# Kernel tuning notes

Hardware: AMD Instinct MI355X
Metric: run time of the kernel (lower is better)

## Reference

```python
import jax, jax.numpy as jnp
import numpy as np

V, E, G = 25000, 50000, 1024
D_IN, E_IN, D, EH = 74, 12, 64, 128
STEPS, S2S, L, NT = 6, 6, 3, 1


def setup_inputs() -> dict:
    key = jax.random.key(0)
    ks = jax.random.split(key, 20)
    p = lambda k, shp: (jax.random.normal(k, shp, jnp.float32) * 0.05)
    return {
        "node_feats": jax.random.normal(ks[0], (V, D_IN), jnp.float32),
        "edge_feats": jax.random.normal(ks[1], (E, E_IN), jnp.float32),
        "src": jax.random.randint(ks[2], (E,), 0, V),
        "dst": jax.random.randint(ks[3], (E,), 0, V),
        "node2graph": jnp.sort(jax.random.randint(ks[4], (V,), 0, G)),
        "W_proj": p(ks[5], (D_IN, D)), "b_proj": jnp.zeros((D,), jnp.float32),
        "W_e1": p(ks[6], (E_IN, EH)), "b_e1": jnp.zeros((EH,), jnp.float32),
        "W_e2": p(ks[7], (EH, D * D)), "b_e2": jnp.zeros((D * D,), jnp.float32),
        "b_conv": jnp.zeros((D,), jnp.float32),
        "gru_W_ih": p(ks[8], (3 * D, D)), "gru_W_hh": p(ks[9], (3 * D, D)),
        "gru_b_ih": jnp.zeros((3 * D,), jnp.float32), "gru_b_hh": jnp.zeros((3 * D,), jnp.float32),
        "lstm_W_ih0": p(ks[10], (4 * D, 2 * D)), "lstm_W_hh0": p(ks[11], (4 * D, D)),
        "lstm_b_ih0": jnp.zeros((4 * D,), jnp.float32), "lstm_b_hh0": jnp.zeros((4 * D,), jnp.float32),
        "lstm_W_ih_r": p(ks[12], (L - 1, 4 * D, D)), "lstm_W_hh_r": p(ks[13], (L - 1, 4 * D, D)),
        "lstm_b_ih_r": jnp.zeros((L - 1, 4 * D), jnp.float32), "lstm_b_hh_r": jnp.zeros((L - 1, 4 * D), jnp.float32),
        "W1": p(ks[14], (2 * D, D)), "b1": jnp.zeros((D,), jnp.float32),
        "bn_gamma": jnp.ones((D,), jnp.float32), "bn_beta": jnp.zeros((D,), jnp.float32),
        "bn_mean": jnp.zeros((D,), jnp.float32), "bn_var": jnp.ones((D,), jnp.float32),
        "W2": p(ks[15], (D, 4 * NT)), "b2": jnp.zeros((4 * NT,), jnp.float32),
    }


def reference(node_feats, edge_feats, src, dst, node2graph,
              W_proj, b_proj, W_e1, b_e1, W_e2, b_e2, b_conv,
              gru_W_ih, gru_W_hh, gru_b_ih, gru_b_hh,
              lstm_W_ih0, lstm_W_hh0, lstm_b_ih0, lstm_b_hh0,
              lstm_W_ih_r, lstm_W_hh_r, lstm_b_ih_r, lstm_b_hh_r,
              W1, b1, bn_gamma, bn_beta, bn_mean, bn_var, W2, b2):
    # --- MPNNGNN: project + ReLU, then NNConv(sum) + ReLU + GRU, x STEPS ---
    h = jax.nn.relu(node_feats @ W_proj + b_proj)                       # (V, D)
    # edge network: per-edge (D,D) mixing matrix (edge_feats constant across steps)
    We = (jax.nn.relu(edge_feats @ W_e1 + b_e1) @ W_e2 + b_e2).reshape(E, D, D)

    def mp_step(hh, _):
        m = jnp.einsum('ed,edo->eo', hh[src], We)                       # per-edge message
        agg = jax.ops.segment_sum(m, dst, num_segments=V) + b_conv      # NNConv sum + bias
        x = jax.nn.relu(agg)
        gi = x @ gru_W_ih.T + gru_b_ih                                  # GRU (torch gate order r,z,n)
        gh = hh @ gru_W_hh.T + gru_b_hh
        ir, iz, inn = jnp.split(gi, 3, axis=-1)
        hr, hz, hn = jnp.split(gh, 3, axis=-1)
        r = jax.nn.sigmoid(ir + hr)
        z = jax.nn.sigmoid(iz + hz)
        n = jnp.tanh(inn + r * hn)
        return (1.0 - z) * n + z * hh, None

    h, _ = jax.lax.scan(mp_step, h, None, length=STEPS)

    # --- Set2Set readout ---
    q_star = jnp.zeros((G, 2 * D), h.dtype)
    hs = jnp.zeros((L, G, D), h.dtype)
    cs = jnp.zeros((L, G, D), h.dtype)
    for _ in range(S2S):
        x = q_star
        nh, nc = [], []
        for l in range(L):                                              # stacked LSTM, seq len 1
            Wih = lstm_W_ih0 if l == 0 else lstm_W_ih_r[l - 1]
            Whh = lstm_W_hh0 if l == 0 else lstm_W_hh_r[l - 1]
            bih = lstm_b_ih0 if l == 0 else lstm_b_ih_r[l - 1]
            bhh = lstm_b_hh0 if l == 0 else lstm_b_hh_r[l - 1]
            gates = x @ Wih.T + bih + hs[l] @ Whh.T + bhh               # torch order i,f,g,o
            i, f, g, o = jnp.split(gates, 4, axis=-1)
            c = jax.nn.sigmoid(f) * cs[l] + jax.nn.sigmoid(i) * jnp.tanh(g)
            hc = jax.nn.sigmoid(o) * jnp.tanh(c)
            nh.append(hc); nc.append(c)
            x = hc
        hs, cs = jnp.stack(nh), jnp.stack(nc)
        q = x                                                           # (G, D)
        e = jnp.sum(h * q[node2graph], axis=-1)                         # (V,) attention logits
        emax = jax.lax.stop_gradient(jax.ops.segment_max(e, node2graph, num_segments=G))
        emax = jnp.where(jnp.isfinite(emax), emax, 0.0)
        ez = jnp.exp(e - emax[node2graph])                              # per-graph softmax
        denom = jax.ops.segment_sum(ez, node2graph, num_segments=G)
        alpha = ez / jnp.maximum(denom[node2graph], 1e-12)
        readout = jax.ops.segment_sum(h * alpha[:, None], node2graph, num_segments=G)
        q_star = jnp.concatenate([q, readout], axis=-1)                 # (G, 2D)

    # --- evidential head: Linear + ReLU + BatchNorm(eval) + Linear ---
    h1 = jax.nn.relu(q_star @ W1 + b1)
    hbn = bn_gamma * (h1 - bn_mean) * jax.lax.rsqrt(bn_var + 1e-5) + bn_beta
    out = hbn @ W2 + b2                                                 # (G, 4*NT)
    means, logl, loga, logb = jnp.split(out, 4, axis=1)
    MINV = 1e-6
    lam = jax.nn.softplus(logl) + MINV
    alp = jax.nn.softplus(loga) + MINV + 1.0
    bet = jax.nn.softplus(logb) + MINV
    return jnp.stack([means, lam, alp, bet], axis=2).reshape(out.shape)
```

## Files before the change

### kernel.cpp

```cpp
#include <hip/hip_runtime.h>
#include <stdint.h>

#define V_N 25000
#define E_N 50000
#define G_N 1024
#define DIN 74
#define EIN 12
#define NSTEPS 6
#define NS2S 6
#define MPAD 50048

typedef unsigned int u32;
typedef unsigned short u16;
typedef __attribute__((ext_vector_type(8))) short bf16x8v;
typedef __attribute__((ext_vector_type(4))) float f32x4v;

typedef __attribute__((address_space(3))) void lds_void;
typedef __attribute__((address_space(1))) void gbl_void;

__device__ __forceinline__ void gload_lds16(const void* g, void* l) {
  __builtin_amdgcn_global_load_lds((gbl_void*)g, (lds_void*)l, 16, 0, 0);
}

__device__ __forceinline__ u16 f2bf(float f) {
  u32 u = __float_as_uint(f);
  u = (u + 0x7fffu + ((u >> 16) & 1u)) >> 16;
  return (u16)u;
}
__device__ __forceinline__ u32 pack2bf(float lo, float hi) {
  return (u32)f2bf(lo) | ((u32)f2bf(hi) << 16);
}
__device__ __forceinline__ float bflo(u32 w){ return __uint_as_float(w << 16); }
__device__ __forceinline__ float bfhi(u32 w){ return __uint_as_float(w & 0xffff0000u); }
__device__ __forceinline__ float sigf(float x){ return 1.f/(1.f + expf(-x)); }
__device__ __forceinline__ float splusf(float x){ return fmaxf(x, 0.f) + log1pf(expf(-fabsf(x))); }

__global__ void prep_kernel(const float* gWih, const float* gWhh,
                            const float* lWih0, const float* lWhh0,
                            const float* lWihr, const float* lWhhr,
                            const float* We2,
                            float* gWihT, float* gWhhT,
                            u32* TW40, u32* TU40, u32* TW4r, u32* TU4r,
                            u16* WbT) {
  int idx = blockIdx.x * 256 + threadIdx.x;
  if (idx < 12288) { int d = idx / 192, r = idx % 192; gWihT[idx] = gWih[r*64 + d]; return; }
  idx -= 12288;
  if (idx < 12288) { int d = idx / 192, r = idx % 192; gWhhT[idx] = gWhh[r*64 + d]; return; }
  idx -= 12288;
  if (idx < 16384) { int q = idx >> 2, j = idx & 3; int k8 = q >> 8, r = q & 255;
                     TW40[idx] = pack2bf(lWih0[r*128 + k8*8 + 2*j], lWih0[r*128 + k8*8 + 2*j + 1]); return; }
  idx -= 16384;
  if (idx < 8192)  { int q = idx >> 2, j = idx & 3; int k8 = q >> 8, r = q & 255;
                     TU40[idx] = pack2bf(lWhh0[r*64 + k8*8 + 2*j], lWhh0[r*64 + k8*8 + 2*j + 1]); return; }
  idx -= 8192;
  if (idx < 16384) { int l = idx >> 13, rem = idx & 8191; int q = rem >> 2, j = rem & 3;
                     int k8 = q >> 8, r = q & 255;
                     TW4r[idx] = pack2bf(lWihr[l*16384 + r*64 + k8*8 + 2*j],
                                         lWihr[l*16384 + r*64 + k8*8 + 2*j + 1]); return; }
  idx -= 16384;
  if (idx < 16384) { int l = idx >> 13, rem = idx & 8191; int q = rem >> 2, j = rem & 3;
                     int k8 = q >> 8, r = q & 255;
                     TU4r[idx] = pack2bf(lWhhr[l*16384 + r*64 + k8*8 + 2*j],
                                         lWhhr[l*16384 + r*64 + k8*8 + 2*j + 1]); return; }
  idx -= 16384;
  { int n = idx / 128, k = idx % 128; WbT[idx] = f2bf(We2[k*4096 + n]); }
}

__global__ void proj_kernel(const float* nf, const float* Wp, const float* bp, float* h) {
  int v = blockIdx.x * 4 + (threadIdx.x >> 6);
  int o = threadIdx.x & 63;
  if (v >= V_N) return;
  float acc = bp[o];
  const float* row = nf + (size_t)v * DIN;
  #pragma unroll 2
  for (int d = 0; d < DIN; ++d) acc += row[d] * Wp[d*64 + o];
  h[(size_t)v*64 + o] = fmaxf(acc, 0.f);
}

__global__ void edgenet_kernel(const float* ef, const float* W1, const float* b1, u16* zb) {
  int e = blockIdx.x * 2 + (threadIdx.x >> 7);
  int k = threadIdx.x & 127;
  float acc = 0.f;
  if (e < E_N) {
    acc = b1[k];
    const float* row = ef + (size_t)e * EIN;
    #pragma unroll
    for (int i = 0; i < EIN; ++i) acc += row[i] * W1[i*128 + k];
    acc = fmaxf(acc, 0.f);
  }
  zb[(size_t)e*128 + k] = f2bf(acc);
}

__global__ __launch_bounds__(512) void fusedmsg_kernel(const u16* zb, const u16* WbT, const float* be2,
                                                       const float* h, const int* src, const int* dst,
                                                       float* agg) {
  __shared__ __align__(16) u16 Bs[2][8192];
  __shared__ float hS[128][66];
  int t = threadIdx.x;
  int e0 = blockIdx.x * 128;
  int w = t >> 6, lane = t & 63;
  int l16 = lane & 15, lh = lane >> 4;

  for (int it = 0; it < 16; ++it) {
    int idx = it * 512 + t;
    int el = idx >> 6, d = idx & 63;
    int e = e0 + el;
    int sv = (e < E_N) ? src[e] : 0;
    hS[el][d] = h[(size_t)sv * 64 + d];
  }

  bf16x8v af[4];
  #pragma unroll
  for (int ks = 0; ks < 4; ++ks)
    af[ks] = *(const bf16x8v*)(zb + (size_t)(e0 + w*16 + l16)*128 + ks*32 + lh*8);

  {
    const char* Bg = (const char*)WbT;
    char* Bl = (char*)Bs[0];
    #pragma unroll
    for (int it = 0; it < 2; ++it) {
      int f = it * 512 + t;
      int r = f >> 4, s = f & 15;
      int gc = s ^ (r & 7);
      gload_lds16(Bg + r*256 + gc*16, Bl + (size_t)(f & ~63) * 16);
    }
  }
  __syncthreads();

  float macc[4][4];
  #pragma unroll
  for (int of = 0; of < 4; ++of)
    #pragma unroll
    for (int r = 0; r < 4; ++r) macc[of][r] = 0.f;

  for (int d = 0; d < 64; ++d) {
    int buf = d & 1;
    if (d < 63) {
      const char* Bg = (const char*)WbT + (size_t)(d + 1) * 16384;
      char* Bl = (char*)Bs[buf ^ 1];
      #pragma unroll
      for (int it = 0; it < 2; ++it) {
        int f = it * 512 + t;
        int r = f >> 4, s = f & 15;
        int gc = s ^ (r & 7);
        gload_lds16(Bg + r*256 + gc*16, Bl + (size_t)(f & ~63) * 16);
      }
    }
    float hv[4];
    #pragma unroll
    for (int r = 0; r < 4; ++r) hv[r] = hS[w*16 + lh*4 + r][d];

    const char* Bb = (const char*)Bs[buf];
    #pragma unroll
    for (int of = 0; of < 4; ++of) {
      float bias = be2[d*64 + of*16 + l16];
      f32x4v c = (f32x4v){bias, bias, bias, bias};
      #pragma unroll
      for (int ks = 0; ks < 4; ++ks) {
        int brow = of*16 + l16;
        int cb = ks*4 + lh;
        bf16x8v bf = *(const bf16x8v*)(Bb + brow*256 + ((cb ^ (brow & 7)) << 4));
        c = __builtin_amdgcn_mfma_f32_16x16x32_bf16(af[ks], bf, c, 0, 0, 0);
      }
      #pragma unroll
      for (int r = 0; r < 4; ++r) macc[of][r] += hv[r] * c[r];
    }
    __syncthreads();
  }

  #pragma unroll
  for (int r = 0; r < 4; ++r) {
    int row = w*16 + lh*4 + r;
    int e = e0 + row;
    if (e < E_N) {
      int dv = dst[e];
      #pragma unroll
      for (int of = 0; of < 4; ++of)
        atomicAdd(&agg[(size_t)dv*64 + of*16 + l16], macc[of][r]);
    }
  }
}

__global__ void gru_kernel(const float* aggc, const float* bconv, const float* WihT, const float* WhhT,
                           const float* bih, const float* bhh, float* h, float* aggz) {
  int wbase = (blockIdx.x * 4 + (threadIdx.x >> 6)) * 4;
  int o = threadIdx.x & 63;
  float xv[4], hv[4];
  #pragma unroll
  for (int n = 0; n < 4; ++n) {
    int v = wbase + n;
    if (v < V_N) { xv[n] = fmaxf(aggc[(size_t)v*64 + o] + bconv[o], 0.f); hv[n] = h[(size_t)v*64 + o]; }
    else { xv[n] = 0.f; hv[n] = 0.f; }
  }
  float ar[4] = {0,0,0,0}, az[4] = {0,0,0,0}, an[4] = {0,0,0,0};
  float br[4] = {0,0,0,0}, bz[4] = {0,0,0,0}, bn2[4] = {0,0,0,0};
  #pragma unroll 4
  for (int d = 0; d < 64; ++d) {
    float wr = WihT[d*192 + o], wz = WihT[d*192 + 64 + o], wn = WihT[d*192 + 128 + o];
    float ur = WhhT[d*192 + o], uz = WhhT[d*192 + 64 + o], un = WhhT[d*192 + 128 + o];
    #pragma unroll
    for (int n = 0; n < 4; ++n) {
      float xd = __shfl(xv[n], d);
      float hd = __shfl(hv[n], d);
      ar[n] += xd*wr; az[n] += xd*wz; an[n] += xd*wn;
      br[n] += hd*ur; bz[n] += hd*uz; bn2[n] += hd*un;
    }
  }
  float b_r = bih[o] + bhh[o], b_z = bih[64+o] + bhh[64+o];
  float bin = bih[128+o], bhn = bhh[128+o];
  #pragma unroll
  for (int n = 0; n < 4; ++n) {
    int v = wbase + n;
    if (v >= V_N) continue;
    float r  = sigf(ar[n] + br[n] + b_r);
    float z  = sigf(az[n] + bz[n] + b_z);
    float nn = tanhf(an[n] + bin + r*(bn2[n] + bhn));
    h[(size_t)v*64 + o] = (1.f - z)*nn + z*hv[n];
    aggz[(size_t)v*64 + o] = 0.f;
  }
}

__global__ void gstart_kernel(const int* n2g, int* gstart) {
  int g = blockIdx.x * 256 + threadIdx.x;
  if (g > G_N) return;
  int lo = 0, hi = V_N;
  while (lo < hi) { int mid = (lo + hi) >> 1; if (n2g[mid] < g) lo = mid + 1; else hi = mid; }
  gstart[g] = lo;
}

__global__ __launch_bounds__(256) void s2s_kernel(const float* h, const int* gstart,
    const uint4* TW40, const uint4* TU40, const uint4* TW4r, const uint4* TU4r,
    const float* bih0, const float* bhh0, const float* bihr, const float* bhhr,
    float* qstar) {
  __shared__ float sq[4][128];
  __shared__ float sx[4][128];
  __shared__ float shs[4][3][64], scs[4][3][64];
  __shared__ float sg[4][256];
  int tt = threadIdx.x;
  int g0blk = blockIdx.x * 4;
  int w = tt >> 6, lane = tt & 63;
  int nstart = gstart[g0blk + w], nend = gstart[g0blk + w + 1];

  for (int i = tt; i < 512; i += 256) ((float*)sq)[i] = 0.f;
  for (int i = tt; i < 768; i += 256) { ((float*)shs)[i] = 0.f; ((float*)scs)[i] = 0.f; }
  __syncthreads();

  for (int iter = 0; iter < NS2S; ++iter) {
    for (int i = tt; i < 512; i += 256) ((float*)sx)[i] = ((float*)sq)[i];
    __syncthreads();

    for (int l = 0; l < 3; ++l) {
      const uint4* TW = (l == 0) ? TW40 : TW4r + (size_t)(l-1) * 2048;
      const uint4* TU = (l == 0) ? TU40 : TU4r + (size_t)(l-1) * 2048;
      const float* bi = (l == 0) ? bih0 : bihr + (l-1)*256;
      const float* bh = (l == 0) ? bhh0 : bhhr + (l-1)*256;
      float bsum = bi[tt] + bh[tt];
      float acc[4] = {bsum, bsum, bsum, bsum};
      if (l == 0) {
        #pragma unroll
        for (int k8 = 0; k8 < 16; ++k8) {
          uint4 u = TW[k8*256 + tt];
          #pragma unroll
          for (int gi = 0; gi < 4; ++gi) {
            const float4 xa = *(const float4*)&sx[gi][k8*8];
            const float4 xb = *(const float4*)&sx[gi][k8*8 + 4];
            acc[gi] += xa.x*bflo(u.x) + xa.y*bfhi(u.x) + xa.z*bflo(u.y) + xa.w*bfhi(u.y)
                     + xb.x*bflo(u.z) + xb.y*bfhi(u.z) + xb.z*bflo(u.w) + xb.w*bfhi(u.w);
          }
        }
      } else {
        #pragma unroll
        for (int k8 = 0; k8 < 8; ++k8) {
          uint4 u = TW[k8*256 + tt];
          #pragma unroll
          for (int gi = 0; gi < 4; ++gi) {
            const float4 xa = *(const float4*)&sx[gi][k8*8];
            const float4 xb = *(const float4*)&sx[gi][k8*8 + 4];
            acc[gi] += xa.x*bflo(u.x) + xa.y*bfhi(u.x) + xa.z*bflo(u.y) + xa.w*bfhi(u.y)
                     + xb.x*bflo(u.z) + xb.y*bfhi(u.z) + xb.z*bflo(u.w) + xb.w*bfhi(u.w);
          }
        }
      }
      #pragma unroll
      for (int k8 = 0; k8 < 8; ++k8) {
        uint4 u = TU[k8*256 + tt];
        #pragma unroll
        for (int gi = 0; gi < 4; ++gi) {
          const float4 ha = *(const float4*)&shs[gi][l][k8*8];
          const float4 hb = *(const float4*)&shs[gi][l][k8*8 + 4];
          acc[gi] += ha.x*bflo(u.x) + ha.y*bfhi(u.x) + ha.z*bflo(u.y) + ha.w*bfhi(u.y)
                   + hb.x*bflo(u.z) + hb.y*bfhi(u.z) + hb.z*bflo(u.w) + hb.w*bfhi(u.w);
        }
      }
      #pragma unroll
      for (int gi = 0; gi < 4; ++gi) sg[gi][tt] = acc[gi];
      __syncthreads();
      {
        int gq = tt >> 6, r = tt & 63;
        float gv_i = sg[gq][r], gv_f = sg[gq][64+r], gv_g = sg[gq][128+r], gv_o = sg[gq][192+r];
        float c = sigf(gv_f)*scs[gq][l][r] + sigf(gv_i)*tanhf(gv_g);
        float hc = sigf(gv_o)*tanhf(c);
        scs[gq][l][r] = c; shs[gq][l][r] = hc; sx[gq][r] = hc;
      }
      __syncthreads();
    }

    {
      float q_l = sx[w][lane];
      float lmax = -3.4e38f;
      int i = nstart;
      for (; i + 1 < nend; i += 2) {
        float h0 = h[(size_t)i*64 + lane];
        float h1 = h[(size_t)(i+1)*64 + lane];
        float v0 = h0 * q_l, v1 = h1 * q_l;
        #pragma unroll
        for (int off = 32; off; off >>= 1) { v0 += __shfl_xor(v0, off); v1 += __shfl_xor(v1, off); }
        lmax = fmaxf(lmax, fmaxf(v0, v1));
      }
      if (i < nend) {
        float h0 = h[(size_t)i*64 + lane];
        float v0 = h0 * q_l;
        #pragma unroll
        for (int off = 32; off; off >>= 1) v0 += __shfl_xor(v0, off);
        lmax = fmaxf(lmax, v0);
      }
      float lsum = 0.f, accv = 0.f;
      i = nstart;
      for (; i + 1 < nend; i += 2) {
        float h0 = h[(size_t)i*64 + lane];
        float h1 = h[(size_t)(i+1)*64 + lane];
        float v0 = h0 * q_l, v1 = h1 * q_l;
        #pragma unroll
        for (int off = 32; off; off >>= 1) { v0 += __shfl_xor(v0, off); v1 += __shfl_xor(v1, off); }
        float e0 = expf(v0 - lmax), e1 = expf(v1 - lmax);
        lsum += e0 + e1; accv += e0*h0 + e1*h1;
      }
      if (i < nend) {
        float h0 = h[(size_t)i*64 + lane];
        float v0 = h0 * q_l;
        #pragma unroll
        for (int off = 32; off; off >>= 1) v0 += __shfl_xor(v0, off);
        float e0 = expf(v0 - lmax);
        lsum += e0; accv += e0*h0;
      }
      sq[w][lane] = sx[w][lane];
      sq[w][64 + lane] = accv / fmaxf(lsum, 1e-12f);
    }
    __syncthreads();
  }

  for (int i = tt; i < 512; i += 256) qstar[(size_t)g0blk * 128 + i] = ((float*)sq)[i];
}

__global__ void head_kernel(const float* qstar, const float* W1, const float* b1,
                            const float* gma, const float* gbe, const float* gme, const float* gva,
                            const float* W2, const float* b2, float* out) {
  __shared__ float hb[4][64];
  int wslot = threadIdx.x >> 6;
  int g = blockIdx.x * 4 + wslot;
  int o = threadIdx.x & 63;
  float acc = b1[o];
  const float* q = qstar + (size_t)g * 128;
  #pragma unroll 4
  for (int k = 0; k < 128; ++k) acc += q[k] * W1[k*64 + o];
  acc = fmaxf(acc, 0.f);
  float hbn = gma[o] * (acc - gme[o]) * rsqrtf(gva[o] + 1e-5f) + gbe[o];
  hb[wslot][o] = hbn;
  __syncthreads();
  if (o < 4) {
    float v = b2[o];
    #pragma unroll 8
    for (int k = 0; k < 64; ++k) v += hb[wslot][k] * W2[k*4 + o];
    float res;
    if (o == 0) res = v;
    else { res = splusf(v) + 1e-6f; if (o == 2) res += 1.f; }
    out[(size_t)g*4 + o] = res;
  }
}

extern "C" void kernel_launch(void* const* d_in, const int* in_sizes, int n_in,
                              void* d_out, int out_size, void* d_ws, size_t ws_size,
                              hipStream_t stream) {
  const float* node_feats = (const float*)d_in[0];
  const float* edge_feats = (const float*)d_in[1];
  const int*   src        = (const int*)d_in[2];
  const int*   dst        = (const int*)d_in[3];
  const int*   n2g        = (const int*)d_in[4];
  const float* W_proj = (const float*)d_in[5];
  const float* b_proj = (const float*)d_in[6];
  const float* W_e1   = (const float*)d_in[7];
  const float* b_e1   = (const float*)d_in[8];
  const float* W_e2   = (const float*)d_in[9];
  const float* b_e2   = (const float*)d_in[10];
  const float* b_conv = (const float*)d_in[11];
  const float* gru_W_ih = (const float*)d_in[12];
  const float* gru_W_hh = (const float*)d_in[13];
  const float* gru_b_ih = (const float*)d_in[14];
  const float* gru_b_hh = (const float*)d_in[15];
  const float* lstm_W_ih0 = (const float*)d_in[16];
  const float* lstm_W_hh0 = (const float*)d_in[17];
  const float* lstm_b_ih0 = (const float*)d_in[18];
  const float* lstm_b_hh0 = (const float*)d_in[19];
  const float* lstm_W_ih_r = (const float*)d_in[20];
  const float* lstm_W_hh_r = (const float*)d_in[21];
  const float* lstm_b_ih_r = (const float*)d_in[22];
  const float* lstm_b_hh_r = (const float*)d_in[23];
  const float* W1 = (const float*)d_in[24];
  const float* b1 = (const float*)d_in[25];
  const float* bn_gamma = (const float*)d_in[26];
  const float* bn_beta  = (const float*)d_in[27];
  const float* bn_mean  = (const float*)d_in[28];
  const float* bn_var   = (const float*)d_in[29];
  const float* W2 = (const float*)d_in[30];
  const float* b2 = (const float*)d_in[31];

  char* ws = (char*)d_ws;
  size_t off = 0;
  auto alloc = [&](size_t n) { size_t c = off; off += (n + 255) & ~(size_t)255; return c; };
  u16*   zb     = (u16*)  (ws + alloc((size_t)MPAD * 128 * 2));
  float* h      = (float*)(ws + alloc((size_t)V_N * 64 * 4));
  float* agg    = (float*)(ws + alloc((size_t)V_N * 64 * 4));
  u16*   WbT    = (u16*)  (ws + alloc((size_t)4096 * 128 * 2));
  float* gWihT  = (float*)(ws + alloc(12288 * 4));
  float* gWhhT  = (float*)(ws + alloc(12288 * 4));
  u32*   TW40   = (u32*)  (ws + alloc(16384 * 4));
  u32*   TU40   = (u32*)  (ws + alloc(8192 * 4));
  u32*   TW4r   = (u32*)  (ws + alloc(16384 * 4));
  u32*   TU4r   = (u32*)  (ws + alloc(16384 * 4));
  int*   gstart = (int*)  (ws + alloc(1025 * 4));
  float* qstar  = (float*)(ws + alloc((size_t)G_N * 128 * 4));
  (void)in_sizes; (void)n_in; (void)out_size; (void)ws_size;

  prep_kernel<<<2368, 256, 0, stream>>>(gru_W_ih, gru_W_hh, lstm_W_ih0, lstm_W_hh0,
                                        lstm_W_ih_r, lstm_W_hh_r, W_e2,
                                        gWihT, gWhhT, TW40, TU40, TW4r, TU4r, WbT);
  proj_kernel<<<6250, 256, 0, stream>>>(node_feats, W_proj, b_proj, h);
  edgenet_kernel<<<MPAD / 2, 256, 0, stream>>>(edge_feats, W_e1, b_e1, zb);
  hipMemsetAsync(agg, 0, (size_t)V_N * 64 * 4, stream);

  for (int st = 0; st < NSTEPS; ++st) {
    fusedmsg_kernel<<<MPAD / 128, 512, 0, stream>>>(zb, WbT, b_e2, h, src, dst, agg);
    gru_kernel<<<1563, 256, 0, stream>>>(agg, b_conv, gWihT, gWhhT, gru_b_ih, gru_b_hh, h, agg);
  }

  gstart_kernel<<<5, 256, 0, stream>>>(n2g, gstart);
  s2s_kernel<<<256, 256, 0, stream>>>(h, gstart, (const uint4*)TW40, (const uint4*)TU40,
                                      (const uint4*)TW4r, (const uint4*)TU4r,
                                      lstm_b_ih0, lstm_b_hh0, lstm_b_ih_r, lstm_b_hh_r, qstar);
  head_kernel<<<256, 256, 0, stream>>>(qstar, W1, b1, bn_gamma, bn_beta, bn_mean, bn_var,
                                       W2, b2, (float*)d_out);
}
```

Baseline: 1.081 ms.

## Retile message kernel to 256 threads with two row fragments; split s2s graphs across waves

The fused NNConv message kernel now uses 256 threads per block, each wave handling 32 edges (two MFMA row fragments) that share the same B fragment read from LDS. Gathered source h is stored in LDS as bf16, and the edge-net bias is staged in LDS. MPAD grows to a multiple of 256 so every block has 128 edges per its 4 waves. Separately, the Set2Set kernel handles 2 graphs per block, with 2 waves splitting each graph's nodes and reducing max/sum through shared memory, doubling the grid. Risks: bf16 h loses precision, higher register pressure, and extra barriers in s2s.

```diff
diff --git a/kernel.cpp b/kernel.cpp
--- a/kernel.cpp
+++ b/kernel.cpp
@@ -8,7 +8,7 @@
 #define EIN 12
 #define NSTEPS 6
 #define NS2S 6
-#define MPAD 50048
+#define MPAD 50176
 
 typedef unsigned int u32;
 typedef unsigned short u16;
@@ -32,6 +32,7 @@
 }
 __device__ __forceinline__ float bflo(u32 w){ return __uint_as_float(w << 16); }
 __device__ __forceinline__ float bfhi(u32 w){ return __uint_as_float(w & 0xffff0000u); }
+__device__ __forceinline__ float bf2f(u16 v){ return __uint_as_float(((u32)v) << 16); }
 __device__ __forceinline__ float sigf(float x){ return 1.f/(1.f + expf(-x)); }
 __device__ __forceinline__ float splusf(float x){ return fmaxf(x, 0.f) + log1pf(expf(-fabsf(x))); }
 
@@ -91,35 +92,41 @@
   zb[(size_t)e*128 + k] = f2bf(acc);
 }
 
-__global__ __launch_bounds__(512) void fusedmsg_kernel(const u16* zb, const u16* WbT, const float* be2,
+__global__ __launch_bounds__(256) void fusedmsg_kernel(const u16* zb, const u16* WbT, const float* be2,
                                                        const float* h, const int* src, const int* dst,
                                                        float* agg) {
   __shared__ __align__(16) u16 Bs[2][8192];
-  __shared__ float hS[128][66];
+  __shared__ u16 hS[128][66];
+  __shared__ float beS[4096];
   int t = threadIdx.x;
   int e0 = blockIdx.x * 128;
   int w = t >> 6, lane = t & 63;
   int l16 = lane & 15, lh = lane >> 4;
 
-  for (int it = 0; it < 16; ++it) {
-    int idx = it * 512 + t;
+  #pragma unroll
+  for (int it = 0; it < 16; ++it) beS[it * 256 + t] = be2[it * 256 + t];
+
+  for (int it = 0; it < 32; ++it) {
+    int idx = it * 256 + t;
     int el = idx >> 6, d = idx & 63;
     int e = e0 + el;
     int sv = (e < E_N) ? src[e] : 0;
-    hS[el][d] = h[(size_t)sv * 64 + d];
-  }
-
-  bf16x8v af[4];
-  #pragma unroll
-  for (int ks = 0; ks < 4; ++ks)
-    af[ks] = *(const bf16x8v*)(zb + (size_t)(e0 + w*16 + l16)*128 + ks*32 + lh*8);
+    hS[el][d] = f2bf(h[(size_t)sv * 64 + d]);
+  }
+
+  bf16x8v af[2][4];
+  #pragma unroll
+  for (int rf = 0; rf < 2; ++rf)
+    #pragma unroll
+    for (int ks = 0; ks < 4; ++ks)
+      af[rf][ks] = *(const bf16x8v*)(zb + (size_t)(e0 + w*32 + rf*16 + l16)*128 + ks*32 + lh*8);
 
   {
     const char* Bg = (const char*)WbT;
     char* Bl = (char*)Bs[0];
     #pragma unroll
-    for (int it = 0; it < 2; ++it) {
-      int f = it * 512 + t;
+    for (int it = 0; it < 4; ++it) {
+      int f = it * 256 + t;
       int r = f >> 4, s = f & 15;
       int gc = s ^ (r & 7);
       gload_lds16(Bg + r*256 + gc*16, Bl + (size_t)(f & ~63) * 16);
@@ -127,11 +134,13 @@
   }
   __syncthreads();
 
-  float macc[4][4];
-  #pragma unroll
-  for (int of = 0; of < 4; ++of)
-    #pragma unroll
-    for (int r = 0; r < 4; ++r) macc[of][r] = 0.f;
+  float macc[2][4][4];
+  #pragma unroll
+  for (int rf = 0; rf < 2; ++rf)
+    #pragma unroll
+    for (int of = 0; of < 4; ++of)
+      #pragma unroll
+      for (int r = 0; r < 4; ++r) macc[rf][of][r] = 0.f;
 
   for (int d = 0; d < 64; ++d) {
     int buf = d & 1;
@@ -139,46 +148,56 @@
       const char* Bg = (const char*)WbT + (size_t)(d + 1) * 16384;
       char* Bl = (char*)Bs[buf ^ 1];
       #pragma unroll
-      for (int it = 0; it < 2; ++it) {
-        int f = it * 512 + t;
+      for (int it = 0; it < 4; ++it) {
+        int f = it * 256 + t;
         int r = f >> 4, s = f & 15;
         int gc = s ^ (r & 7);
         gload_lds16(Bg + r*256 + gc*16, Bl + (size_t)(f & ~63) * 16);
       }
     }
-    float hv[4];
-    #pragma unroll
-    for (int r = 0; r < 4; ++r) hv[r] = hS[w*16 + lh*4 + r][d];
+    float hv[2][4];
+    #pragma unroll
+    for (int rf = 0; rf < 2; ++rf)
+      #pragma unroll
+      for (int r = 0; r < 4; ++r)
+        hv[rf][r] = bf2f(hS[w*32 + rf*16 + lh*4 + r][d]);
 
     const char* Bb = (const char*)Bs[buf];
     #pragma unroll
     for (int of = 0; of < 4; ++of) {
-      float bias = be2[d*64 + of*16 + l16];
-      f32x4v c = (f32x4v){bias, bias, bias, bias};
+      float bias = beS[d*64 + of*16 + l16];
+      f32x4v c0 = (f32x4v){bias, bias, bias, bias};
+      f32x4v c1 = c0;
       #pragma unroll
       for (int ks = 0; ks < 4; ++ks) {
         int brow = of*16 + l16;
         int cb = ks*4 + lh;
         bf16x8v bf = *(const bf16x8v*)(Bb + brow*256 + ((cb ^ (brow & 7)) << 4));
-        c = __builtin_amdgcn_mfma_f32_16x16x32_bf16(af[ks], bf, c, 0, 0, 0);
-      }
-      #pragma unroll
-      for (int r = 0; r < 4; ++r) macc[of][r] += hv[r] * c[r];
+        c0 = __builtin_amdgcn_mfma_f32_16x16x32_bf16(af[0][ks], bf, c0, 0, 0, 0);
+        c1 = __builtin_amdgcn_mfma_f32_16x16x32_bf16(af[1][ks], bf, c1, 0, 0, 0);
+      }
+      #pragma unroll
+      for (int r = 0; r < 4; ++r) {
+        macc[0][of][r] += hv[0][r] * c0[r];
+        macc[1][of][r] += hv[1][r] * c1[r];
+      }
     }
     __syncthreads();
   }
 
   #pragma unroll
-  for (int r = 0; r < 4; ++r) {
-    int row = w*16 + lh*4 + r;
-    int e = e0 + row;
-    if (e < E_N) {
-      int dv = dst[e];
-      #pragma unroll
-      for (int of = 0; of < 4; ++of)
-        atomicAdd(&agg[(size_t)dv*64 + of*16 + l16], macc[of][r]);
-    }
-  }
+  for (int rf = 0; rf < 2; ++rf)
+    #pragma unroll
+    for (int r = 0; r < 4; ++r) {
+      int row = w*32 + rf*16 + lh*4 + r;
+      int e = e0 + row;
+      if (e < E_N) {
+        int dv = dst[e];
+        #pragma unroll
+        for (int of = 0; of < 4; ++of)
+          atomicAdd(&agg[(size_t)dv*64 + of*16 + l16], macc[rf][of][r]);
+      }
+    }
 }
 
 __global__ void gru_kernel(const float* aggc, const float* bconv, const float* WihT, const float* WhhT,
@@ -232,21 +251,23 @@
     const uint4* TW40, const uint4* TU40, const uint4* TW4r, const uint4* TU4r,
     const float* bih0, const float* bhh0, const float* bihr, const float* bhhr,
     float* qstar) {
-  __shared__ float sq[4][128];
-  __shared__ float sx[4][128];
-  __shared__ float shs[4][3][64], scs[4][3][64];
-  __shared__ float sg[4][256];
+  __shared__ float sq[2][128];
+  __shared__ float sx[2][128];
+  __shared__ float shs[2][3][64], scs[2][3][64];
+  __shared__ float sg[2][256];
+  __shared__ float sred[2][2][66];
   int tt = threadIdx.x;
-  int g0blk = blockIdx.x * 4;
+  int g0blk = blockIdx.x * 2;
   int w = tt >> 6, lane = tt & 63;
-  int nstart = gstart[g0blk + w], nend = gstart[g0blk + w + 1];
-
-  for (int i = tt; i < 512; i += 256) ((float*)sq)[i] = 0.f;
-  for (int i = tt; i < 768; i += 256) { ((float*)shs)[i] = 0.f; ((float*)scs)[i] = 0.f; }
+  int gsl = w >> 1, wsub = w & 1;
+  int nstart = gstart[g0blk + gsl], nend = gstart[g0blk + gsl + 1];
+
+  if (tt < 256) { ((float*)sq)[tt] = 0.f; }
+  for (int i = tt; i < 384; i += 256) { ((float*)shs)[i] = 0.f; ((float*)scs)[i] = 0.f; }
   __syncthreads();
 
   for (int iter = 0; iter < NS2S; ++iter) {
-    for (int i = tt; i < 512; i += 256) ((float*)sx)[i] = ((float*)sq)[i];
+    ((float*)sx)[tt] = ((float*)sq)[tt];
     __syncthreads();
 
     for (int l = 0; l < 3; ++l) {
@@ -255,47 +276,55 @@
       const float* bi = (l == 0) ? bih0 : bihr + (l-1)*256;
       const float* bh = (l == 0) ? bhh0 : bhhr + (l-1)*256;
       float bsum = bi[tt] + bh[tt];
-      float acc[4] = {bsum, bsum, bsum, bsum};
+      float acc0 = bsum, acc1 = bsum;
       if (l == 0) {
         #pragma unroll
         for (int k8 = 0; k8 < 16; ++k8) {
           uint4 u = TW[k8*256 + tt];
-          #pragma unroll
-          for (int gi = 0; gi < 4; ++gi) {
-            const float4 xa = *(const float4*)&sx[gi][k8*8];
-            const float4 xb = *(const float4*)&sx[gi][k8*8 + 4];
-            acc[gi] += xa.x*bflo(u.x) + xa.y*bfhi(u.x) + xa.z*bflo(u.y) + xa.w*bfhi(u.y)
-                     + xb.x*bflo(u.z) + xb.y*bfhi(u.z) + xb.z*bflo(u.w) + xb.w*bfhi(u.w);
-          }
+          const float4 xa0 = *(const float4*)&sx[0][k8*8];
+          const float4 xb0 = *(const float4*)&sx[0][k8*8 + 4];
+          const float4 xa1 = *(const float4*)&sx[1][k8*8];
+          const float4 xb1 = *(const float4*)&sx[1][k8*8 + 4];
+          float w0=bflo(u.x),w1=bfhi(u.x),w2=bflo(u.y),w3=bfhi(u.y);
+          float w4=bflo(u.z),w5=bfhi(u.z),w6=bflo(u.w),w7=bfhi(u.w);
+          acc0 += xa0.x*w0 + xa0.y*w1 + xa0.z*w2 + xa0.w*w3
+                + xb0.x*w4 + xb0.y*w5 + xb0.z*w6 + xb0.w*w7;
+          acc1 += xa1.x*w0 + xa1.y*w1 + xa1.z*w2 + xa1.w*w3
+                + xb1.x*w4 + xb1.y*w5 + xb1.z*w6 + xb1.w*w7;
         }
       } else {
         #pragma unroll
         for (int k8 = 0; k8 < 8; ++k8) {
           uint4 u = TW[k8*256 + tt];
-          #pragma unroll
-          for (int gi = 0; gi < 4; ++gi) {
-            const float4 xa = *(const float4*)&sx[gi][k8*8];
-            const float4 xb = *(const float4*)&sx[gi][k8*8 + 4];
-            acc[gi] += xa.x*bflo(u.x) + xa.y*bfhi(u.x) + xa.z*bflo(u.y) + xa.w*bfhi(u.y)
-                     + xb.x*bflo(u.z) + xb.y*bfhi(u.z) + xb.z*bflo(u.w) + xb.w*bfhi(u.w);
-          }
+          const float4 xa0 = *(const float4*)&sx[0][k8*8];
+          const float4 xb0 = *(const float4*)&sx[0][k8*8 + 4];
+          const float4 xa1 = *(const float4*)&sx[1][k8*8];
+          const float4 xb1 = *(const float4*)&sx[1][k8*8 + 4];
+          float w0=bflo(u.x),w1=bfhi(u.x),w2=bflo(u.y),w3=bfhi(u.y);
+          float w4=bflo(u.z),w5=bfhi(u.z),w6=bflo(u.w),w7=bfhi(u.w);
+          acc0 += xa0.x*w0 + xa0.y*w1 + xa0.z*w2 + xa0.w*w3
+                + xb0.x*w4 + xb0.y*w5 + xb0.z*w6 + xb0.w*w7;
+          acc1 += xa1.x*w0 + xa1.y*w1 + xa1.z*w2 + xa1.w*w3
+                + xb1.x*w4 + xb1.y*w5 + xb1.z*w6 + xb1.w*w7;
         }
       }
       #pragma unroll
       for (int k8 = 0; k8 < 8; ++k8) {
         uint4 u = TU[k8*256 + tt];
-        #pragma unroll
-        for (int gi = 0; gi < 4; ++gi) {
-          const float4 ha = *(const float4*)&shs[gi][l][k8*8];
-          const float4 hb = *(const float4*)&shs[gi][l][k8*8 + 4];
-          acc[gi] += ha.x*bflo(u.x) + ha.y*bfhi(u.x) + ha.z*bflo(u.y) + ha.w*bfhi(u.y)
-                   + hb.x*bflo(u.z) + hb.y*bfhi(u.z) + hb.z*bflo(u.w) + hb.w*bfhi(u.w);
-        }
-      }
-      #pragma unroll
-      for (int gi = 0; gi < 4; ++gi) sg[gi][tt] = acc[gi];
+        const float4 ha0 = *(const float4*)&shs[0][l][k8*8];
+        const float4 hb0 = *(const float4*)&shs[0][l][k8*8 + 4];
+        const float4 ha1 = *(const float4*)&shs[1][l][k8*8];
+        const float4 hb1 = *(const float4*)&shs[1][l][k8*8 + 4];
+        float w0=bflo(u.x),w1=bfhi(u.x),w2=bflo(u.y),w3=bfhi(u.y);
+        float w4=bflo(u.z),w5=bfhi(u.z),w6=bflo(u.w),w7=bfhi(u.w);
+        acc0 += ha0.x*w0 + ha0.y*w1 + ha0.z*w2 + ha0.w*w3
+              + hb0.x*w4 + hb0.y*w5 + hb0.z*w6 + hb0.w*w7;
+        acc1 += ha1.x*w0 + ha1.y*w1 + ha1.z*w2 + ha1.w*w3
+              + hb1.x*w4 + hb1.y*w5 + hb1.z*w6 + hb1.w*w7;
+      }
+      sg[0][tt] = acc0; sg[1][tt] = acc1;
       __syncthreads();
-      {
+      if (tt < 128) {
         int gq = tt >> 6, r = tt & 63;
         float gv_i = sg[gq][r], gv_f = sg[gq][64+r], gv_g = sg[gq][128+r], gv_o = sg[gq][192+r];
         float c = sigf(gv_f)*scs[gq][l][r] + sigf(gv_i)*tanhf(gv_g);
@@ -306,12 +335,12 @@
     }
 
     {
-      float q_l = sx[w][lane];
+      float q_l = sx[gsl][lane];
       float lmax = -3.4e38f;
-      int i = nstart;
-      for (; i + 1 < nend; i += 2) {
+      int i = nstart + wsub;
+      for (; i + 2 < nend; i += 4) {
         float h0 = h[(size_t)i*64 + lane];
-        float h1 = h[(size_t)(i+1)*64 + lane];
+        float h1 = h[(size_t)(i+2)*64 + lane];
         float v0 = h0 * q_l, v1 = h1 * q_l;
         #pragma unroll
         for (int off = 32; off; off >>= 1) { v0 += __shfl_xor(v0, off); v1 += __shfl_xor(v1, off); }
@@ -324,15 +353,18 @@
         for (int off = 32; off; off >>= 1) v0 += __shfl_xor(v0, off);
         lmax = fmaxf(lmax, v0);
       }
+      if (lane == 0) sred[gsl][wsub][64] = lmax;
+      __syncthreads();
+      float gmax = fmaxf(sred[gsl][0][64], sred[gsl][1][64]);
       float lsum = 0.f, accv = 0.f;
-      i = nstart;
-      for (; i + 1 < nend; i += 2) {
+      i = nstart + wsub;
+      for (; i + 2 < nend; i += 4) {
         float h0 = h[(size_t)i*64 + lane];
-        float h1 = h[(size_t)(i+1)*64 + lane];
+        float h1 = h[(size_t)(i+2)*64 + lane];
         float v0 = h0 * q_l, v1 = h1 * q_l;
         #pragma unroll
         for (int off = 32; off; off >>= 1) { v0 += __shfl_xor(v0, off); v1 += __shfl_xor(v1, off); }
-        float e0 = expf(v0 - lmax), e1 = expf(v1 - lmax);
+        float e0 = expf(v0 - gmax), e1 = expf(v1 - gmax);
         lsum += e0 + e1; accv += e0*h0 + e1*h1;
       }
       if (i < nend) {
@@ -340,16 +372,24 @@
         float v0 = h0 * q_l;
         #pragma unroll
         for (int off = 32; off; off >>= 1) v0 += __shfl_xor(v0, off);
-        float e0 = expf(v0 - lmax);
+        float e0 = expf(v0 - gmax);
         lsum += e0; accv += e0*h0;
       }
-      sq[w][lane] = sx[w][lane];
-      sq[w][64 + lane] = accv / fmaxf(lsum, 1e-12f);
-    }
-    __syncthreads();
-  }
-
-  for (int i = tt; i < 512; i += 256) qstar[(size_t)g0blk * 128 + i] = ((float*)sq)[i];
+      sred[gsl][wsub][lane] = accv;
+      if (lane == 0) sred[gsl][wsub][65] = lsum;
+      __syncthreads();
+      if (tt < 128) {
+        int gq = tt >> 6, r = tt & 63;
+        float den = sred[gq][0][65] + sred[gq][1][65];
+        float ro = (sred[gq][0][r] + sred[gq][1][r]) / fmaxf(den, 1e-12f);
+        sq[gq][r] = sx[gq][r];
+        sq[gq][64 + r] = ro;
+      }
+      __syncthreads();
+    }
+  }
+
+  qstar[(size_t)g0blk * 128 + tt] = ((float*)sq)[tt];
 }
 
 __global__ void head_kernel(const float* qstar, const float* W1, const float* b1,
@@ -439,12 +479,12 @@
   hipMemsetAsync(agg, 0, (size_t)V_N * 64 * 4, stream);
 
   for (int st = 0; st < NSTEPS; ++st) {
-    fusedmsg_kernel<<<MPAD / 128, 512, 0, stream>>>(zb, WbT, b_e2, h, src, dst, agg);
+    fusedmsg_kernel<<<MPAD / 128, 256, 0, stream>>>(zb, WbT, b_e2, h, src, dst, agg);
     gru_kernel<<<1563, 256, 0, stream>>>(agg, b_conv, gWihT, gWhhT, gru_b_ih, gru_b_hh, h, agg);
   }
 
   gstart_kernel<<<5, 256, 0, stream>>>(n2g, gstart);
-  s2s_kernel<<<256, 256, 0, stream>>>(h, gstart, (const uint4*)TW40, (const uint4*)TU40,
+  s2s_kernel<<<512, 256, 0, stream>>>(h, gstart, (const uint4*)TW40, (const uint4*)TU40,
                                       (const uint4*)TW4r, (const uint4*)TU4r,
                                       lstm_b_ih0, lstm_b_hh0, lstm_b_ih_r, lstm_b_hh_r, qstar);
   head_kernel<<<256, 256, 0, stream>>>(qstar, W1, b1, bn_gamma, bn_beta, bn_mean, bn_var,
```

Result: slower. 1.140 ms (+5.5%).
